# Kernel tuning notes

Hardware: AMD Instinct MI355X
Metric: run time of the kernel (lower is better)

Reference implementation:

```python
import jax, jax.numpy as jnp
import numpy as np


def setup_inputs() -> dict:
    key = jax.random.key(0)
    ks = jax.random.split(key, 6)
    B, Cx, Cf, Ch, H, W = 4, 512, 512, 256, 64, 64
    return {
        "query_features": jax.random.normal(ks[0], (B, Cx, H, W), dtype=jnp.float32),
        "reference_features": jax.random.normal(ks[1], (B, Cf, H, W), dtype=jnp.float32),
        "Wq": jax.random.normal(ks[2], (Ch, Cx), dtype=jnp.float32) * (1.0 / np.sqrt(Cx)),
        "bq": jax.random.normal(ks[3], (Ch,), dtype=jnp.float32) * 0.02,
        "Wk": jax.random.normal(ks[4], (Ch, Cf), dtype=jnp.float32) * (1.0 / np.sqrt(Cf)),
        "bk": jax.random.normal(ks[5], (Ch,), dtype=jnp.float32) * 0.02,
    }


def reference(query_features, reference_features, Wq, bq, Wk, bk):
    # 1x1 convs == per-pixel linear projections over channels
    Q = jnp.einsum('bchw,oc->bohw', query_features, Wq) + bq[None, :, None, None]
    K = jnp.einsum('bchw,oc->bohw', reference_features, Wk) + bk[None, :, None, None]
    B, Cf, H2, W2 = reference_features.shape
    H1, W1 = Q.shape[2], Q.shape[3]
    V = reference_features.reshape(B, Cf, H2 * W2)            # b c p
    # unscaled QK^T over hidden channels: [b, h1, w1, h2*w2]
    scores = jnp.einsum('bcij,bckl->bijkl', Q, K).reshape(B, H1, W1, H2 * W2)
    attn = jax.nn.softmax(scores, axis=-1)
    out = jnp.einsum('bijp,bcp->bcij', attn, V)               # [b, Cf, h1, w1]
    return out
```

## Files before the change

### kernel.cpp

```cpp
#include <hip/hip_runtime.h>
#include <hip/hip_bf16.h>
#include <hip/hip_fp16.h>

typedef _Float16 half8 __attribute__((ext_vector_type(8)));
typedef _Float16 half4v __attribute__((ext_vector_type(4)));
typedef float f4 __attribute__((ext_vector_type(4)));
typedef float f16v __attribute__((ext_vector_type(16)));
typedef short short8 __attribute__((ext_vector_type(8)));
typedef int i4 __attribute__((ext_vector_type(4)));

#define P_SZ 4096
#define CH 256
#define CIN 512
#define CV 512
#define KVB 32

__device__ __forceinline__ unsigned short f2bf(float f) {
  unsigned u = __float_as_uint(f);
  unsigned r = u + 0x7fffu + ((u >> 16) & 1u);
  return (unsigned short)(r >> 16);
}
__device__ __forceinline__ float bf2f(unsigned short h) {
  return __uint_as_float(((unsigned)h) << 16);
}

__device__ __forceinline__ void gload16(const void* g, void* l) {
  __builtin_amdgcn_global_load_lds(
      (const __attribute__((address_space(1))) unsigned int*)g,
      (__attribute__((address_space(3))) unsigned int*)l, 16, 0, 0);
}

__global__ __launch_bounds__(256) void vconv_kernel(const float* __restrict__ in,
                                                    _Float16* __restrict__ outv) {
  const size_t i = (size_t)blockIdx.x * 256 + threadIdx.x;
  const f4 x = ((const f4*)in)[i];
  half4v h;
  h[0] = (_Float16)x[0]; h[1] = (_Float16)x[1];
  h[2] = (_Float16)x[2]; h[3] = (_Float16)x[3];
  const int pq = (int)(i & 1023);
  const int ch = (int)((i >> 10) & 511);
  const int b  = (int)(i >> 19);
  const int p0 = pq * 4;
  const size_t idx = (size_t)b * 2097152 + (size_t)(p0 >> 5) * 16384
                   + (size_t)((p0 >> 3) & 3) * 4096 + ch * 8 + (p0 & 7);
  *(half4v*)(outv + idx) = h;
}

__global__ __launch_bounds__(512) void proj_kernel(
    const float* __restrict__ Xq, const float* __restrict__ Wq, const float* __restrict__ bq,
    const float* __restrict__ Xk, const float* __restrict__ Wk, const float* __restrict__ bk,
    _Float16* __restrict__ Qout, _Float16* __restrict__ Kout) {
  const int which = blockIdx.z;
  const float* __restrict__ X = which ? Xk : Xq;
  const float* __restrict__ W = which ? Wk : Wq;
  const float* __restrict__ bias = which ? bk : bq;
  _Float16* __restrict__ out = which ? Kout : Qout;

  const int b = blockIdx.y;
  const int p0 = blockIdx.x * 64;
  const int tid = threadIdx.x;
  const int w = tid >> 6, l = tid & 63;
  const int wp = w >> 2, wo = w & 3;
  const int lr = l & 15, lg = l >> 4;

  const float* __restrict__ Xb = X + (size_t)b * CIN * P_SZ;

  f4 acc[2][4];
  #pragma unroll
  for (int m = 0; m < 2; ++m)
    #pragma unroll
    for (int n = 0; n < 4; ++n) acc[m][n] = (f4){0.f, 0.f, 0.f, 0.f};

  const int prow0 = p0 + wp * 32 + lr;

  #pragma unroll 1
  for (int kc = 0; kc < CIN; kc += 32) {
    short8 ah[2], al[2];
    #pragma unroll
    for (int m = 0; m < 2; ++m) {
      const float* xp = Xb + (size_t)(kc + lg * 8) * P_SZ + (prow0 + m * 16);
      #pragma unroll
      for (int i = 0; i < 8; ++i) {
        float xv = xp[(size_t)i * P_SZ];
        unsigned short h = f2bf(xv);
        ah[m][i] = (short)h;
        al[m][i] = (short)f2bf(xv - bf2f(h));
      }
    }
    short8 bh[4], bl[4];
    #pragma unroll
    for (int n = 0; n < 4; ++n) {
      const float* wr = W + (size_t)(wo * 64 + n * 16 + lr) * CIN + kc + lg * 8;
      #pragma unroll
      for (int i = 0; i < 8; ++i) {
        float wv = wr[i];
        unsigned short h = f2bf(wv);
        bh[n][i] = (short)h;
        bl[n][i] = (short)f2bf(wv - bf2f(h));
      }
    }
    #pragma unroll
    for (int m = 0; m < 2; ++m)
      #pragma unroll
      for (int n = 0; n < 4; ++n) {
        acc[m][n] = __builtin_amdgcn_mfma_f32_16x16x32_bf16(ah[m], bh[n], acc[m][n], 0, 0, 0);
        acc[m][n] = __builtin_amdgcn_mfma_f32_16x16x32_bf16(ah[m], bl[n], acc[m][n], 0, 0, 0);
        acc[m][n] = __builtin_amdgcn_mfma_f32_16x16x32_bf16(al[m], bh[n], acc[m][n], 0, 0, 0);
      }
  }

  #pragma unroll
  for (int n = 0; n < 4; ++n) {
    const int o = wo * 64 + n * 16 + lr;
    const float bv = bias[o];
    #pragma unroll
    for (int m = 0; m < 2; ++m) {
      #pragma unroll
      for (int j = 0; j < 4; ++j) {
        const int p = p0 + wp * 32 + m * 16 + lg * 4 + j;
        const _Float16 val = (_Float16)(acc[m][n][j] + bv);
        if (which == 0) {
          out[((size_t)b * P_SZ + p) * CH + o] = val;
        } else {
          out[(size_t)b * 1048576 + (size_t)(p >> 5) * 8192
              + (size_t)(o >> 3) * 256 + (p & 31) * 8 + (o & 7)] = val;
        }
      }
    }
  }
}

template <int NSEG, bool DIRECT>
__global__ __launch_bounds__(512, 2) void attn_kernel(
    const _Float16* __restrict__ Qg, const _Float16* __restrict__ Kt,
    const _Float16* __restrict__ Vt, float* __restrict__ Opart,
    float* __restrict__ Mp, float* __restrict__ Lp, float* __restrict__ Og) {
  __shared__ char K_l[3][16384];
  __shared__ char V_l[3][32768];

  constexpr int nt = (P_SZ / NSEG) / KVB;
  int b, qt, seg;
  if (NSEG == 2) {
    const int g = blockIdx.x & 7;
    b = g >> 1; seg = g & 1; qt = blockIdx.x >> 3;
  } else {
    b = blockIdx.x & 3; seg = 0; qt = blockIdx.x >> 2;
  }

  const int tid = threadIdx.x;
  const int w = tid >> 6, l = tid & 63;
  const int hi = l >> 5, l31 = l & 31;
  const int wq = w >> 1, half = w & 1;

  const char* Kb = (const char*)Kt + (size_t)b * 2097152 + (size_t)seg * nt * 16384;
  const char* Vb = (const char*)Vt + (size_t)b * 4194304 + (size_t)seg * nt * 32768;

#define STAGE(BUF, T) do { \
    const char* ksrc = Kb + (size_t)(T) * 16384; \
    const char* vsrc = Vb + (size_t)(T) * 32768; \
    gload16(ksrc + tid * 16,         &K_l[BUF][w * 1024]); \
    gload16(ksrc + 8192 + tid * 16,  &K_l[BUF][8192 + w * 1024]); \
    gload16(vsrc + tid * 16,         &V_l[BUF][w * 1024]); \
    gload16(vsrc + 8192 + tid * 16,  &V_l[BUF][8192 + w * 1024]); \
    gload16(vsrc + 16384 + tid * 16, &V_l[BUF][16384 + w * 1024]); \
    gload16(vsrc + 24576 + tid * 16, &V_l[BUF][24576 + w * 1024]); \
  } while (0)

  half8 qf[16];
  {
    const char* qrow = (const char*)Qg +
        ((size_t)b * P_SZ + qt * 128 + wq * 32 + l31) * 512;
    #pragma unroll
    for (int m = 0; m < 16; ++m) qf[m] = *(const half8*)(qrow + m * 32 + hi * 16);
  }

  f16v acc[8];
  #pragma unroll
  for (int n = 0; n < 8; ++n)
    acc[n] = (f16v){0,0,0,0, 0,0,0,0, 0,0,0,0, 0,0,0,0};

  float m_run = -1e30f, lsum = 0.f;
  const int kread = hi * 512 + l31 * 16;
  const int vread = hi * 8192 + half * 4096 + l31 * 16;

  STAGE(0, 0); STAGE(1, 1);
  asm volatile("s_waitcnt vmcnt(6)" ::: "memory");
  asm volatile("s_barrier" ::: "memory");
  __builtin_amdgcn_sched_barrier(0);

  int bufc = 0;
  #pragma unroll 1
  for (int t = 0; t < nt; ++t) {
    const char* kb = &K_l[bufc][0] + kread;
    f16v s = (f16v){0,0,0,0, 0,0,0,0, 0,0,0,0, 0,0,0,0};
    __builtin_amdgcn_s_setprio(1);
    #pragma unroll
    for (int m = 0; m < 16; ++m) {
      half8 kf = *(const half8*)(kb + m * 1024);
      s = __builtin_amdgcn_mfma_f32_32x32x16_f16(kf, qf[m], s, 0, 0, 0);
    }
    __builtin_amdgcn_s_setprio(0);

    float x0 = fmaxf(s[0], s[8]),  x1 = fmaxf(s[1], s[9]);
    float x2 = fmaxf(s[2], s[10]), x3 = fmaxf(s[3], s[11]);
    float x4 = fmaxf(s[4], s[12]), x5 = fmaxf(s[5], s[13]);
    float x6 = fmaxf(s[6], s[14]), x7 = fmaxf(s[7], s[15]);
    x0 = fmaxf(x0, x4); x1 = fmaxf(x1, x5); x2 = fmaxf(x2, x6); x3 = fmaxf(x3, x7);
    float pm = fmaxf(fmaxf(x0, x1), fmaxf(x2, x3));
    pm = fmaxf(pm, __shfl_xor(pm, 32));
    if (__any(pm > m_run + 10.f)) {
      const float mnew = fmaxf(m_run, pm);
      const float al = __expf(m_run - mnew);
      const int alb = __float_as_int(al);
      #pragma unroll
      for (int r = 0; r < 16; ++r) {
        const int cr = (r & 3) + 8 * (r >> 2);
        const float ar = __int_as_float(
            __builtin_amdgcn_ds_bpermute(cr * 4 + hi * 16, alb));
        #pragma unroll
        for (int n = 0; n < 8; ++n) acc[n][r] *= ar;
      }
      lsum *= al;
      m_run = mnew;
    }
    float p[16], psum;
    #pragma unroll
    for (int r = 0; r < 16; ++r) p[r] = __expf(s[r] - m_run);
    {
      float a0 = (p[0] + p[1]) + (p[2] + p[3]);
      float a1 = (p[4] + p[5]) + (p[6] + p[7]);
      float a2 = (p[8] + p[9]) + (p[10] + p[11]);
      float a3 = (p[12] + p[13]) + (p[14] + p[15]);
      psum = (a0 + a1) + (a2 + a3);
      psum += __shfl_xor(psum, 32);
    }
    lsum += psum;

    const int c0 = __builtin_bit_cast(int, __builtin_amdgcn_cvt_pkrtz(p[0], p[1]));
    const int c1 = __builtin_bit_cast(int, __builtin_amdgcn_cvt_pkrtz(p[2], p[3]));
    const int c2 = __builtin_bit_cast(int, __builtin_amdgcn_cvt_pkrtz(p[4], p[5]));
    const int c3 = __builtin_bit_cast(int, __builtin_amdgcn_cvt_pkrtz(p[6], p[7]));
    const int c4 = __builtin_bit_cast(int, __builtin_amdgcn_cvt_pkrtz(p[8], p[9]));
    const int c5 = __builtin_bit_cast(int, __builtin_amdgcn_cvt_pkrtz(p[10], p[11]));
    const int c6 = __builtin_bit_cast(int, __builtin_amdgcn_cvt_pkrtz(p[12], p[13]));
    const int c7 = __builtin_bit_cast(int, __builtin_amdgcn_cvt_pkrtz(p[14], p[15]));
    const int c0x = __shfl_xor(c0, 32), c1x = __shfl_xor(c1, 32);
    const int c2x = __shfl_xor(c2, 32), c3x = __shfl_xor(c3, 32);
    const int c4x = __shfl_xor(c4, 32), c5x = __shfl_xor(c5, 32);
    const int c6x = __shfl_xor(c6, 32), c7x = __shfl_xor(c7, 32);
    i4 w0v, w1v;
    w0v[0] = hi ? c2x : c0;  w0v[1] = hi ? c3x : c1;
    w0v[2] = hi ? c2  : c0x; w0v[3] = hi ? c3  : c1x;
    w1v[0] = hi ? c6x : c4;  w1v[1] = hi ? c7x : c5;
    w1v[2] = hi ? c6  : c4x; w1v[3] = hi ? c7  : c5x;
    const half8 pa0 = __builtin_bit_cast(half8, w0v);
    const half8 pa1 = __builtin_bit_cast(half8, w1v);

    const int bufs = bufc == 0 ? 2 : bufc - 1;
    if (t + 2 < nt) STAGE(bufs, t + 2);

    const char* vb = &V_l[bufc][0] + vread;
    __builtin_amdgcn_s_setprio(1);
    #pragma unroll
    for (int n = 0; n < 8; ++n) {
      half8 v0 = *(const half8*)(vb + n * 512);
      acc[n] = __builtin_amdgcn_mfma_f32_32x32x16_f16(pa0, v0, acc[n], 0, 0, 0);
      half8 v1 = *(const half8*)(vb + 16384 + n * 512);
      acc[n] = __builtin_amdgcn_mfma_f32_32x32x16_f16(pa1, v1, acc[n], 0, 0, 0);
    }
    __builtin_amdgcn_s_setprio(0);

    if (t + 2 < nt) { asm volatile("s_waitcnt vmcnt(6)" ::: "memory"); }
    else            { asm volatile("s_waitcnt vmcnt(0)" ::: "memory"); }
    asm volatile("s_barrier" ::: "memory");
    __builtin_amdgcn_sched_barrier(0);
    bufc = bufc == 2 ? 0 : bufc + 1;
  }
#undef STAGE

  const int qg0 = qt * 128 + wq * 32;
  if (!DIRECT) {
    float* Ob = Opart + (((size_t)seg * 4 + b) * P_SZ + qg0) * 512 + half * 256 + l31;
    #pragma unroll
    for (int n = 0; n < 8; ++n) {
      #pragma unroll
      for (int r = 0; r < 16; ++r) {
        const int q = (r & 3) + 8 * (r >> 2) + 4 * hi;
        Ob[(size_t)q * 512 + n * 32] = acc[n][r];
      }
    }
    if (half == 0 && l < 32) {
      const size_t mi = ((size_t)seg * 4 + b) * P_SZ + qg0 + l31;
      Mp[mi] = m_run; Lp[mi] = lsum;
    }
  } else {
    float linv[16];
    const int lb = __float_as_int(lsum);
    #pragma unroll
    for (int r = 0; r < 16; ++r) {
      const int cr = (r & 3) + 8 * (r >> 2);
      const float lq = __int_as_float(__builtin_amdgcn_ds_bpermute(cr * 4 + hi * 16, lb));
      linv[r] = 1.f / lq;
    }
    #pragma unroll
    for (int n = 0; n < 8; ++n) {
      #pragma unroll
      for (int r = 0; r < 16; ++r) {
        const int q = (r & 3) + 8 * (r >> 2) + 4 * hi;
        Og[((size_t)b * CV + half * 256 + n * 32 + l31) * P_SZ + qg0 + q] =
            acc[n][r] * linv[r];
      }
    }
  }
}

template <int NSEG>
__global__ __launch_bounds__(256) void combine_kernel(
    const float* __restrict__ Opart, const float* __restrict__ Mp,
    const float* __restrict__ Lp, float* __restrict__ Og) {
  __shared__ float T[64][65];
  const int bx = blockIdx.x;
  const int ct = bx & 7, qt = (bx >> 3) & 63, b = bx >> 9;
  const int tid = threadIdx.x;
  {
    const int qi = tid >> 2, cj = tid & 3;
    const int q = qt * 64 + qi;
    const size_t mibase = (size_t)b * P_SZ + q;
    float M = -1e30f;
    #pragma unroll
    for (int s = 0; s < NSEG; ++s) M = fmaxf(M, Mp[(size_t)s * 4 * P_SZ + mibase]);
    float L = 0.f;
    f4 o0 = {0,0,0,0}, o1 = {0,0,0,0}, o2 = {0,0,0,0}, o3 = {0,0,0,0};
    #pragma unroll
    for (int s = 0; s < NSEG; ++s) {
      const float wgt = __expf(Mp[(size_t)s * 4 * P_SZ + mibase] - M);
      L += wgt * Lp[(size_t)s * 4 * P_SZ + mibase];
      const float* src = Opart + (((size_t)s * 4 + b) * P_SZ + q) * 512 + ct * 64 + cj * 16;
      o0 += wgt * ((const f4*)src)[0];
      o1 += wgt * ((const f4*)src)[1];
      o2 += wgt * ((const f4*)src)[2];
      o3 += wgt * ((const f4*)src)[3];
    }
    const float inv = 1.f / L;
    #pragma unroll
    for (int e = 0; e < 4; ++e) {
      T[qi][cj * 16 + e]      = o0[e] * inv;
      T[qi][cj * 16 + 4 + e]  = o1[e] * inv;
      T[qi][cj * 16 + 8 + e]  = o2[e] * inv;
      T[qi][cj * 16 + 12 + e] = o3[e] * inv;
    }
  }
  __syncthreads();
  const int ci = tid >> 2, qj = tid & 3;
  #pragma unroll
  for (int i = 0; i < 4; ++i) {
    f4 v;
    #pragma unroll
    for (int e = 0; e < 4; ++e) v[e] = T[qj * 16 + i * 4 + e][ci];
    *(f4*)&Og[((size_t)b * CV + ct * 64 + ci) * P_SZ + qt * 64 + qj * 16 + i * 4] = v;
  }
}

extern "C" void kernel_launch(void* const* d_in, const int* in_sizes, int n_in,
                              void* d_out, int out_size, void* d_ws, size_t ws_size,
                              hipStream_t stream) {
  const float* x  = (const float*)d_in[0];
  const float* f  = (const float*)d_in[1];
  const float* Wq = (const float*)d_in[2];
  const float* bq = (const float*)d_in[3];
  const float* Wk = (const float*)d_in[4];
  const float* bk = (const float*)d_in[5];
  float* out = (float*)d_out;

  char* ws = (char*)d_ws;
  _Float16* Qf = (_Float16*)ws;
  _Float16* Kf = (_Float16*)(ws + ((size_t)8 << 20));
  _Float16* Vf = (_Float16*)(ws + ((size_t)16 << 20));
  float* Mp    = (float*)(ws + ((size_t)32 << 20));
  float* Lp    = (float*)(ws + ((size_t)32 << 20) + 262144);
  float* Opart = (float*)(ws + ((size_t)33 << 20));

  vconv_kernel<<<dim3(8192), dim3(256), 0, stream>>>(f, Vf);
  proj_kernel<<<dim3(64, 4, 2), dim3(512), 0, stream>>>(x, Wq, bq, f, Wk, bk, Qf, Kf);

  const size_t need2 = ((size_t)33 << 20) + ((size_t)64 << 20);
  const size_t need1 = ((size_t)33 << 20) + ((size_t)32 << 20);
  if (ws_size >= need2) {
    attn_kernel<2, false><<<dim3(256), dim3(512), 0, stream>>>(Qf, Kf, Vf, Opart, Mp, Lp, nullptr);
    combine_kernel<2><<<dim3(2048), dim3(256), 0, stream>>>(Opart, Mp, Lp, out);
  } else if (ws_size >= need1) {
    attn_kernel<1, false><<<dim3(128), dim3(512), 0, stream>>>(Qf, Kf, Vf, Opart, Mp, Lp, nullptr);
    combine_kernel<1><<<dim3(2048), dim3(256), 0, stream>>>(Opart, Mp, Lp, out);
  } else {
    attn_kernel<1, true><<<dim3(128), dim3(512), 0, stream>>>(Qf, Kf, Vf, nullptr, nullptr, nullptr, out);
  }
}
```

Baseline: 261.5 us.

## Precompute split-bf16 weights, fold log2e into Q, swizzle K, store partials as bf16

Adds a small kernel that converts Wq/Wk once per call into hi/lo bf16 pairs, with log2(e) folded into Wq and bq, so the projection loads ready-made short8 vectors instead of converting in its inner loop. The attention softmax then uses exp2f directly. K rows are stored with a permuted (swizzled) order, which removes the cross-half shuffles used to build the P operand for the PV MFMA. Split-K partial outputs are written and read as bf16 instead of fp32, halving that traffic. In exchange there is an extra kernel launch and reduced precision in the partial outputs, and the rescale threshold is loosened.

```diff
diff --git a/kernel.cpp b/kernel.cpp
--- a/kernel.cpp
+++ b/kernel.cpp
@@ -7,6 +7,7 @@
 typedef float f4 __attribute__((ext_vector_type(4)));
 typedef float f16v __attribute__((ext_vector_type(16)));
 typedef short short8 __attribute__((ext_vector_type(8)));
+typedef unsigned short us8 __attribute__((ext_vector_type(8)));
 typedef int i4 __attribute__((ext_vector_type(4)));
 
 #define P_SZ 4096
@@ -14,6 +15,7 @@
 #define CIN 512
 #define CV 512
 #define KVB 32
+#define L2E 1.4426950408889634f
 
 __device__ __forceinline__ unsigned short f2bf(float f) {
   unsigned u = __float_as_uint(f);
@@ -28,6 +30,18 @@
   __builtin_amdgcn_global_load_lds(
       (const __attribute__((address_space(1))) unsigned int*)g,
       (__attribute__((address_space(3))) unsigned int*)l, 16, 0, 0);
+}
+
+__global__ __launch_bounds__(256) void wconv_kernel(
+    const float* __restrict__ Wq, const float* __restrict__ Wk,
+    short* __restrict__ Wh, short* __restrict__ Wl) {
+  const int i = blockIdx.x * 256 + threadIdx.x;
+  const int which = i >> 17;
+  const int j = i & 131071;
+  const float w = which ? Wk[j] : Wq[j] * L2E;
+  const unsigned short h = f2bf(w);
+  Wh[i] = (short)h;
+  Wl[i] = (short)f2bf(w - bf2f(h));
 }
 
 __global__ __launch_bounds__(256) void vconv_kernel(const float* __restrict__ in,
@@ -47,14 +61,15 @@
 }
 
 __global__ __launch_bounds__(512) void proj_kernel(
-    const float* __restrict__ Xq, const float* __restrict__ Wq, const float* __restrict__ bq,
-    const float* __restrict__ Xk, const float* __restrict__ Wk, const float* __restrict__ bk,
+    const float* __restrict__ Xq, const float* __restrict__ bq,
+    const float* __restrict__ Xk, const float* __restrict__ bk,
+    const short* __restrict__ Wh, const short* __restrict__ Wl,
     _Float16* __restrict__ Qout, _Float16* __restrict__ Kout) {
   const int which = blockIdx.z;
   const float* __restrict__ X = which ? Xk : Xq;
-  const float* __restrict__ W = which ? Wk : Wq;
   const float* __restrict__ bias = which ? bk : bq;
   _Float16* __restrict__ out = which ? Kout : Qout;
+  const float bscale = which ? 1.f : L2E;
 
   const int b = blockIdx.y;
   const int p0 = blockIdx.x * 64;
@@ -64,6 +79,8 @@
   const int lr = l & 15, lg = l >> 4;
 
   const float* __restrict__ Xb = X + (size_t)b * CIN * P_SZ;
+  const short* __restrict__ Whb = Wh + (size_t)which * 131072;
+  const short* __restrict__ Wlb = Wl + (size_t)which * 131072;
 
   f4 acc[2][4];
   #pragma unroll
@@ -90,14 +107,9 @@
     short8 bh[4], bl[4];
     #pragma unroll
     for (int n = 0; n < 4; ++n) {
-      const float* wr = W + (size_t)(wo * 64 + n * 16 + lr) * CIN + kc + lg * 8;
-      #pragma unroll
-      for (int i = 0; i < 8; ++i) {
-        float wv = wr[i];
-        unsigned short h = f2bf(wv);
-        bh[n][i] = (short)h;
-        bl[n][i] = (short)f2bf(wv - bf2f(h));
-      }
+      const size_t wi = (size_t)(wo * 64 + n * 16 + lr) * CIN + kc + lg * 8;
+      bh[n] = *(const short8*)(Whb + wi);
+      bl[n] = *(const short8*)(Wlb + wi);
     }
     #pragma unroll
     for (int m = 0; m < 2; ++m)
@@ -112,7 +124,7 @@
   #pragma unroll
   for (int n = 0; n < 4; ++n) {
     const int o = wo * 64 + n * 16 + lr;
-    const float bv = bias[o];
+    const float bv = bias[o] * bscale;
     #pragma unroll
     for (int m = 0; m < 2; ++m) {
       #pragma unroll
@@ -122,8 +134,10 @@
         if (which == 0) {
           out[((size_t)b * P_SZ + p) * CH + o] = val;
         } else {
+          const int kk = p & 31;
+          const int kswz = (kk & 19) | ((kk & 4) << 1) | ((kk & 8) >> 1);
           out[(size_t)b * 1048576 + (size_t)(p >> 5) * 8192
-              + (size_t)(o >> 3) * 256 + (p & 31) * 8 + (o & 7)] = val;
+              + (size_t)(o >> 3) * 256 + kswz * 8 + (o & 7)] = val;
         }
       }
     }
@@ -133,7 +147,7 @@
 template <int NSEG, bool DIRECT>
 __global__ __launch_bounds__(512, 2) void attn_kernel(
     const _Float16* __restrict__ Qg, const _Float16* __restrict__ Kt,
-    const _Float16* __restrict__ Vt, float* __restrict__ Opart,
+    const _Float16* __restrict__ Vt, unsigned short* __restrict__ Opart,
     float* __restrict__ Mp, float* __restrict__ Lp, float* __restrict__ Og) {
   __shared__ char K_l[3][16384];
   __shared__ char V_l[3][32768];
@@ -208,9 +222,9 @@
     x0 = fmaxf(x0, x4); x1 = fmaxf(x1, x5); x2 = fmaxf(x2, x6); x3 = fmaxf(x3, x7);
     float pm = fmaxf(fmaxf(x0, x1), fmaxf(x2, x3));
     pm = fmaxf(pm, __shfl_xor(pm, 32));
-    if (__any(pm > m_run + 10.f)) {
+    if (__any(pm > m_run + 12.f)) {
       const float mnew = fmaxf(m_run, pm);
-      const float al = __expf(m_run - mnew);
+      const float al = exp2f(m_run - mnew);
       const int alb = __float_as_int(al);
       #pragma unroll
       for (int r = 0; r < 16; ++r) {
@@ -225,7 +239,7 @@
     }
     float p[16], psum;
     #pragma unroll
-    for (int r = 0; r < 16; ++r) p[r] = __expf(s[r] - m_run);
+    for (int r = 0; r < 16; ++r) p[r] = exp2f(s[r] - m_run);
     {
       float a0 = (p[0] + p[1]) + (p[2] + p[3]);
       float a1 = (p[4] + p[5]) + (p[6] + p[7]);
@@ -236,23 +250,15 @@
     }
     lsum += psum;
 
-    const int c0 = __builtin_bit_cast(int, __builtin_amdgcn_cvt_pkrtz(p[0], p[1]));
-    const int c1 = __builtin_bit_cast(int, __builtin_amdgcn_cvt_pkrtz(p[2], p[3]));
-    const int c2 = __builtin_bit_cast(int, __builtin_amdgcn_cvt_pkrtz(p[4], p[5]));
-    const int c3 = __builtin_bit_cast(int, __builtin_amdgcn_cvt_pkrtz(p[6], p[7]));
-    const int c4 = __builtin_bit_cast(int, __builtin_amdgcn_cvt_pkrtz(p[8], p[9]));
-    const int c5 = __builtin_bit_cast(int, __builtin_amdgcn_cvt_pkrtz(p[10], p[11]));
-    const int c6 = __builtin_bit_cast(int, __builtin_amdgcn_cvt_pkrtz(p[12], p[13]));
-    const int c7 = __builtin_bit_cast(int, __builtin_amdgcn_cvt_pkrtz(p[14], p[15]));
-    const int c0x = __shfl_xor(c0, 32), c1x = __shfl_xor(c1, 32);
-    const int c2x = __shfl_xor(c2, 32), c3x = __shfl_xor(c3, 32);
-    const int c4x = __shfl_xor(c4, 32), c5x = __shfl_xor(c5, 32);
-    const int c6x = __shfl_xor(c6, 32), c7x = __shfl_xor(c7, 32);
     i4 w0v, w1v;
-    w0v[0] = hi ? c2x : c0;  w0v[1] = hi ? c3x : c1;
-    w0v[2] = hi ? c2  : c0x; w0v[3] = hi ? c3  : c1x;
-    w1v[0] = hi ? c6x : c4;  w1v[1] = hi ? c7x : c5;
-    w1v[2] = hi ? c6  : c4x; w1v[3] = hi ? c7  : c5x;
+    w0v[0] = __builtin_bit_cast(int, __builtin_amdgcn_cvt_pkrtz(p[0], p[1]));
+    w0v[1] = __builtin_bit_cast(int, __builtin_amdgcn_cvt_pkrtz(p[2], p[3]));
+    w0v[2] = __builtin_bit_cast(int, __builtin_amdgcn_cvt_pkrtz(p[4], p[5]));
+    w0v[3] = __builtin_bit_cast(int, __builtin_amdgcn_cvt_pkrtz(p[6], p[7]));
+    w1v[0] = __builtin_bit_cast(int, __builtin_amdgcn_cvt_pkrtz(p[8], p[9]));
+    w1v[1] = __builtin_bit_cast(int, __builtin_amdgcn_cvt_pkrtz(p[10], p[11]));
+    w1v[2] = __builtin_bit_cast(int, __builtin_amdgcn_cvt_pkrtz(p[12], p[13]));
+    w1v[3] = __builtin_bit_cast(int, __builtin_amdgcn_cvt_pkrtz(p[14], p[15]));
     const half8 pa0 = __builtin_bit_cast(half8, w0v);
     const half8 pa1 = __builtin_bit_cast(half8, w1v);
 
@@ -280,13 +286,14 @@
 
   const int qg0 = qt * 128 + wq * 32;
   if (!DIRECT) {
-    float* Ob = Opart + (((size_t)seg * 4 + b) * P_SZ + qg0) * 512 + half * 256 + l31;
+    unsigned short* Ob = Opart +
+        (((size_t)seg * 4 + b) * P_SZ + qg0) * 512 + half * 256 + l31;
     #pragma unroll
     for (int n = 0; n < 8; ++n) {
       #pragma unroll
       for (int r = 0; r < 16; ++r) {
         const int q = (r & 3) + 8 * (r >> 2) + 4 * hi;
-        Ob[(size_t)q * 512 + n * 32] = acc[n][r];
+        Ob[(size_t)q * 512 + n * 32] = f2bf(acc[n][r]);
       }
     }
     if (half == 0 && l < 32) {
@@ -316,7 +323,7 @@
 
 template <int NSEG>
 __global__ __launch_bounds__(256) void combine_kernel(
-    const float* __restrict__ Opart, const float* __restrict__ Mp,
+    const unsigned short* __restrict__ Opart, const float* __restrict__ Mp,
     const float* __restrict__ Lp, float* __restrict__ Og) {
   __shared__ float T[64][65];
   const int bx = blockIdx.x;
@@ -330,25 +337,26 @@
     #pragma unroll
     for (int s = 0; s < NSEG; ++s) M = fmaxf(M, Mp[(size_t)s * 4 * P_SZ + mibase]);
     float L = 0.f;
-    f4 o0 = {0,0,0,0}, o1 = {0,0,0,0}, o2 = {0,0,0,0}, o3 = {0,0,0,0};
+    float o[16];
+    #pragma unroll
+    for (int e = 0; e < 16; ++e) o[e] = 0.f;
     #pragma unroll
     for (int s = 0; s < NSEG; ++s) {
-      const float wgt = __expf(Mp[(size_t)s * 4 * P_SZ + mibase] - M);
+      const float wgt = exp2f(Mp[(size_t)s * 4 * P_SZ + mibase] - M);
       L += wgt * Lp[(size_t)s * 4 * P_SZ + mibase];
-      const float* src = Opart + (((size_t)s * 4 + b) * P_SZ + q) * 512 + ct * 64 + cj * 16;
-      o0 += wgt * ((const f4*)src)[0];
-      o1 += wgt * ((const f4*)src)[1];
-      o2 += wgt * ((const f4*)src)[2];
-      o3 += wgt * ((const f4*)src)[3];
+      const unsigned short* src = Opart +
+          (((size_t)s * 4 + b) * P_SZ + q) * 512 + ct * 64 + cj * 16;
+      const us8 ua = ((const us8*)src)[0];
+      const us8 ub = ((const us8*)src)[1];
+      #pragma unroll
+      for (int e = 0; e < 8; ++e) {
+        o[e]     += wgt * bf2f(ua[e]);
+        o[8 + e] += wgt * bf2f(ub[e]);
+      }
     }
     const float inv = 1.f / L;
     #pragma unroll
-    for (int e = 0; e < 4; ++e) {
-      T[qi][cj * 16 + e]      = o0[e] * inv;
-      T[qi][cj * 16 + 4 + e]  = o1[e] * inv;
-      T[qi][cj * 16 + 8 + e]  = o2[e] * inv;
-      T[qi][cj * 16 + 12 + e] = o3[e] * inv;
-    }
+    for (int e = 0; e < 16; ++e) T[qi][cj * 16 + e] = o[e] * inv;
   }
   __syncthreads();
   const int ci = tid >> 2, qj = tid & 3;
@@ -377,14 +385,17 @@
   _Float16* Kf = (_Float16*)(ws + ((size_t)8 << 20));
   _Float16* Vf = (_Float16*)(ws + ((size_t)16 << 20));
   float* Mp    = (float*)(ws + ((size_t)32 << 20));
-  float* Lp    = (float*)(ws + ((size_t)32 << 20) + 262144);
-  float* Opart = (float*)(ws + ((size_t)33 << 20));
-
+  float* Lp    = (float*)(ws + ((size_t)32 << 20) + (256 << 10));
+  short* Wh    = (short*)(ws + ((size_t)32 << 20) + (512 << 10));
+  short* Wl    = (short*)(ws + ((size_t)33 << 20));
+  unsigned short* Opart = (unsigned short*)(ws + ((size_t)34 << 20));
+
+  wconv_kernel<<<dim3(1024), dim3(256), 0, stream>>>(Wq, Wk, Wh, Wl);
   vconv_kernel<<<dim3(8192), dim3(256), 0, stream>>>(f, Vf);
-  proj_kernel<<<dim3(64, 4, 2), dim3(512), 0, stream>>>(x, Wq, bq, f, Wk, bk, Qf, Kf);
-
-  const size_t need2 = ((size_t)33 << 20) + ((size_t)64 << 20);
-  const size_t need1 = ((size_t)33 << 20) + ((size_t)32 << 20);
+  proj_kernel<<<dim3(64, 4, 2), dim3(512), 0, stream>>>(x, bq, f, bk, Wh, Wl, Qf, Kf);
+
+  const size_t need2 = ((size_t)34 << 20) + ((size_t)32 << 20);
+  const size_t need1 = ((size_t)34 << 20) + ((size_t)16 << 20);
   if (ws_size >= need2) {
     attn_kernel<2, false><<<dim3(256), dim3(512), 0, stream>>>(Qf, Kf, Vf, Opart, Mp, Lp, nullptr);
     combine_kernel<2><<<dim3(2048), dim3(256), 0, stream>>>(Opart, Mp, Lp, out);
```

Result: slower. 269.5 us (+3.1%).
